# Kernel optimization log

Hardware: AMD Instinct MI355X
Metric: run time of the kernel (lower is better)

## Reference

```python
import jax, jax.numpy as jnp
import numpy as np

HIDDEN = 1024
HEADS = 16
HEAD_DIM = HIDDEN // HEADS  # 64; softmax scale uses head_dim per SeqAttention(hidden_size=head_dim)


def setup_inputs() -> dict:
    key = jax.random.key(0)
    ks = jax.random.split(key, 7)
    B, M = 2, 2048
    s = 1.0 / np.sqrt(HIDDEN)
    return {
        "query": jax.random.normal(ks[0], (B, M, HIDDEN), jnp.float32),
        "key": jax.random.normal(ks[1], (B, M, HIDDEN), jnp.float32),
        "value": jax.random.normal(ks[2], (B, M, HIDDEN), jnp.float32),
        "Wq": jax.random.normal(ks[3], (HIDDEN, HIDDEN), jnp.float32) * s,
        "Wk": jax.random.normal(ks[4], (HIDDEN, HIDDEN), jnp.float32) * s,
        "Wv": jax.random.normal(ks[5], (HIDDEN, HIDDEN), jnp.float32) * s,
        "Wo": jax.random.normal(ks[6], (HIDDEN, HIDDEN), jnp.float32) * s,
    }


def _split_heads(x):
    # [B, T, H*D] -> [B, H, T, D]
    B, T, _ = x.shape
    return x.reshape(B, T, HEADS, HEAD_DIM).transpose(0, 2, 1, 3)


def reference(query, key, value, Wq, Wk, Wv, Wo):
    # nn.Linear(bias=False): y = x @ W.T
    q = _split_heads(query @ Wq.T)  # [B,H,M,D]
    k = _split_heads(key @ Wk.T)    # [B,H,N,D]
    v = _split_heads(value @ Wv.T)  # [B,H,N,D]
    scale = 1.0 / jnp.sqrt(jnp.asarray(HEAD_DIM, q.dtype))
    attn = jnp.einsum("bhmd,bhnd->bhmn", q, k) * scale
    attn = jax.nn.softmax(attn, axis=-1)
    out = jnp.einsum("bhmn,bhnd->bhmd", attn, v)  # [B,H,M,D]
    B, H, M, D = out.shape
    out = out.transpose(0, 2, 1, 3).reshape(B, M, H * D)
    return out @ Wo.T
```

## Files before the change

kernel.cpp:

```cpp
#include <hip/hip_runtime.h>

typedef __bf16 bf16;
typedef __bf16 bf16x2 __attribute__((ext_vector_type(2)));
typedef __bf16 bf16x8 __attribute__((ext_vector_type(8)));
typedef float  f32x4  __attribute__((ext_vector_type(4)));
typedef float  f32x16 __attribute__((ext_vector_type(16)));
typedef unsigned int u32;
typedef unsigned int u32x4 __attribute__((ext_vector_type(4)));

typedef __attribute__((address_space(1))) unsigned int gu32;
typedef __attribute__((address_space(3))) unsigned int lu32;

__device__ __forceinline__ void llds16(const void* g, void* l) {
  __builtin_amdgcn_global_load_lds((gu32*)g, (lu32*)l, 16, 0, 0);
}

__device__ __forceinline__ void cvt8(const float* __restrict__ src,
                                     bf16* __restrict__ dst, int i) {
  const float4* s4 = (const float4*)src;
  float4 a = s4[i * 2 + 0];
  float4 c = s4[i * 2 + 1];
  bf16x8 o;
  o[0] = (bf16)a.x; o[1] = (bf16)a.y; o[2] = (bf16)a.z; o[3] = (bf16)a.w;
  o[4] = (bf16)c.x; o[5] = (bf16)c.y; o[6] = (bf16)c.z; o[7] = (bf16)c.w;
  ((bf16x8*)dst)[i] = o;
}

__global__ __launch_bounds__(256) void cvt_bf16(const float* __restrict__ src,
                                                bf16* __restrict__ dst, int n8) {
  int i = blockIdx.x * blockDim.x + threadIdx.x;
  if (i < n8) cvt8(src, dst, i);
}

__global__ __launch_bounds__(256) void cvt_all(const float* __restrict__ w0,
                                               const float* __restrict__ w1,
                                               const float* __restrict__ w2,
                                               const float* __restrict__ w3,
                                               const float* __restrict__ x0,
                                               const float* __restrict__ x1,
                                               const float* __restrict__ x2,
                                               bf16* __restrict__ wdst,
                                               bf16* __restrict__ xdst) {
  const int b = blockIdx.x;
  if (b < 2048) {
    const int which = b >> 9;
    const float* src = (which == 0) ? w0 : (which == 1) ? w1 : (which == 2) ? w2 : w3;
    const int i = (b & 511) * 256 + threadIdx.x;
    cvt8(src, wdst + (size_t)which * (1u << 20), i);
  } else {
    const int b2 = b - 2048;
    const int which = b2 >> 11;
    const float* src = (which == 0) ? x0 : (which == 1) ? x1 : x2;
    const int i = (b2 & 2047) * 256 + threadIdx.x;
    cvt8(src, xdst + (size_t)which * (4u << 20), i);
  }
}

__global__ __launch_bounds__(256) void gemm_qkv(const bf16* __restrict__ A0,
                                                const bf16* __restrict__ A1,
                                                const bf16* __restrict__ A2,
                                                const bf16* __restrict__ Wb,
                                                bf16* __restrict__ qb,
                                                bf16* __restrict__ kb,
                                                bf16* __restrict__ vb,
                                                int zoff) {
  constexpr int K = 1024, BM = 128, BN = 128, BK = 32, NT = K / BK;
  __shared__ bf16 Alds[2][BM * BK];
  __shared__ bf16 Blds[2][BN * BK];
  const int t = threadIdx.x, w = t >> 6, l = t & 63;
  const int lr = l & 15, lg = l >> 4;
  const int bm = blockIdx.x * BM, bn = blockIdx.y * BN;
  const int z = blockIdx.z + zoff;
  const bf16* A = (z == 0) ? A0 : (z == 1) ? A1 : A2;
  const bf16* W = Wb + (size_t)z * (1u << 20);
  const int wm = (w >> 1) * 64, wn = (w & 1) * 64;

  f32x4 acc[4][4] = {};

  auto stage = [&](int buf, int kt) {
    const int k0 = kt * BK;
#pragma unroll
    for (int i = 0; i < 2; ++i) {
      int idx = i * 256 + t;
      int row = idx >> 2, kb2 = (idx & 3) * 16;
      llds16((const char*)A + ((size_t)(bm + row) * K + k0) * 2 + kb2,
             (char*)(&Alds[buf][0]) + (i * 4 + w) * 1024);
    }
#pragma unroll
    for (int i = 0; i < 2; ++i) {
      int idx = i * 256 + t;
      int row = idx >> 2, kb2 = (idx & 3) * 16;
      llds16((const char*)W + ((size_t)(bn + row) * K + k0) * 2 + kb2,
             (char*)(&Blds[buf][0]) + (i * 4 + w) * 1024);
    }
  };

  stage(0, 0);
  for (int kt = 0; kt < NT; ++kt) {
    __syncthreads();
    if (kt + 1 < NT) stage((kt + 1) & 1, kt + 1);
    const int cur = kt & 1;
    bf16x8 af[4], bfr[4];
#pragma unroll
    for (int i = 0; i < 4; ++i)
      af[i] = *(const bf16x8*)(&Alds[cur][(wm + i * 16 + lr) * BK + lg * 8]);
#pragma unroll
    for (int j = 0; j < 4; ++j)
      bfr[j] = *(const bf16x8*)(&Blds[cur][(wn + j * 16 + lr) * BK + lg * 8]);
    __builtin_amdgcn_s_setprio(1);
#pragma unroll
    for (int i = 0; i < 4; ++i)
#pragma unroll
      for (int j = 0; j < 4; ++j)
        acc[i][j] = __builtin_amdgcn_mfma_f32_16x16x32_bf16(af[i], bfr[j], acc[i][j], 0, 0, 0);
    __builtin_amdgcn_s_setprio(0);
  }

  bf16* Cout = (z == 0) ? qb : (z == 1) ? kb : vb;
  const float osc = (z == 0) ? 0.1803368801f : 1.0f;
#pragma unroll
  for (int i = 0; i < 4; ++i) {
#pragma unroll
    for (int j = 0; j < 4; ++j) {
#pragma unroll
      for (int r = 0; r < 4; ++r) {
        const int gm = bm + wm + i * 16 + lg * 4 + r;
        const int n  = bn + wn + j * 16 + lr;
        const int b = gm >> 11, m = gm & 2047;
        const int h = n >> 6, d = n & 63;
        const size_t off = (z < 2)
            ? ((size_t)((b * 16 + h) * 2048 + m) * 64 + d)
            : ((size_t)((b * 16 + h) * 64 + d) * 2048 + m);
        Cout[off] = (bf16)(acc[i][j][r] * osc);
      }
    }
  }
}

__global__ __launch_bounds__(256) void gemm_out(const bf16* __restrict__ A,
                                                const bf16* __restrict__ Bw,
                                                float* __restrict__ Cout) {
  constexpr int N = 1024, K = 1024;
  constexpr int BM = 128, BN = 64, BK = 32;
  __shared__ bf16 Alds[2][BM * BK];
  __shared__ bf16 Blds[2][BN * BK];
  const int t = threadIdx.x;
  const int w = t >> 6, l = t & 63;
  const int lr = l & 15, lg = l >> 4;
  const int bm = blockIdx.x * BM, bn = blockIdx.y * BN;
  const int wm = (w >> 1) * 64, wn = (w & 1) * 32;

  f32x4 acc[4][2] = {};

  auto stage = [&](int buf, int kt) {
    const int k0 = kt * BK;
#pragma unroll
    for (int i = 0; i < 2; ++i) {
      int idx = i * 256 + t;
      int row = idx >> 2, kb = (idx & 3) * 16;
      const char* g = (const char*)A + ((size_t)(bm + row) * K + k0) * 2 + kb;
      llds16(g, (char*)(&Alds[buf][0]) + (i * 4 + w) * 1024);
    }
    {
      int row = t >> 2, kb = (t & 3) * 16;
      const char* g = (const char*)Bw + ((size_t)(bn + row) * K + k0) * 2 + kb;
      llds16(g, (char*)(&Blds[buf][0]) + w * 1024);
    }
  };

  stage(0, 0);
  constexpr int NT = K / BK;
  for (int kt = 0; kt < NT; ++kt) {
    __syncthreads();
    if (kt + 1 < NT) stage((kt + 1) & 1, kt + 1);
    const int cur = kt & 1;
    bf16x8 af[4], bfr[2];
#pragma unroll
    for (int i = 0; i < 4; ++i)
      af[i] = *(const bf16x8*)(&Alds[cur][(wm + i * 16 + lr) * BK + lg * 8]);
#pragma unroll
    for (int j = 0; j < 2; ++j)
      bfr[j] = *(const bf16x8*)(&Blds[cur][(wn + j * 16 + lr) * BK + lg * 8]);
    __builtin_amdgcn_s_setprio(1);
#pragma unroll
    for (int i = 0; i < 4; ++i)
#pragma unroll
      for (int j = 0; j < 2; ++j)
        acc[i][j] = __builtin_amdgcn_mfma_f32_16x16x32_bf16(af[i], bfr[j], acc[i][j], 0, 0, 0);
    __builtin_amdgcn_s_setprio(0);
  }

#pragma unroll
  for (int i = 0; i < 4; ++i)
#pragma unroll
    for (int j = 0; j < 2; ++j)
#pragma unroll
      for (int r = 0; r < 4; ++r) {
        const int gm = bm + wm + i * 16 + lg * 4 + r;
        const int n  = bn + wn + j * 16 + lr;
        Cout[(size_t)gm * N + n] = acc[i][j][r];
      }
}

__global__ __launch_bounds__(128) void attn_fwd(const bf16* __restrict__ Qb,
                                                const bf16* __restrict__ Kb,
                                                const bf16* __restrict__ Vt,
                                                bf16* __restrict__ Out) {
  constexpr int Mlen = 2048, KVB = 64, NTT = Mlen / KVB;
  __shared__ bf16 Klds[2][KVB * 64];
  __shared__ bf16 Vlds[2][64 * KVB];
  const int t = threadIdx.x, w = t >> 6, l = t & 63;
  const int l31 = l & 31, hi = l >> 5;
  const int orig = blockIdx.y * 32 + blockIdx.x;
  const int wg = (orig & 7) * 128 + (orig >> 3);
  const int bh = wg >> 5;
  const int qr = (wg & 31) * 64 + w * 32;
  const int key = (l31 & 7) << 4;

  const bf16* qbase = Qb + ((size_t)bh * Mlen + qr + l31) * 64;
  bf16x8 qf[4];
#pragma unroll
  for (int dks = 0; dks < 4; ++dks)
    qf[dks] = *(const bf16x8*)(qbase + dks * 16 + hi * 8);

  f32x16 acco0 = {}, acco1 = {};
  float lsum = 0.f;

  const char* kTile0 = (const char*)Kb + (size_t)bh * Mlen * 64 * 2;
  const char* vBase  = (const char*)Vt + (size_t)bh * 64 * Mlen * 2;

  auto stageKV = [&](int buf, int tile) {
    const int kv0 = tile * KVB;
#pragma unroll
    for (int i = 0; i < 4; ++i) {
      int idx = i * 128 + t;
      int L = idx * 16;
      int row = L >> 7;
      int inner = (L & 127) ^ ((row & 7) << 4);
      llds16(kTile0 + (size_t)(kv0 + row) * 128 + inner,
             (char*)(&Klds[buf][0]) + (i * 2 + w) * 1024);
    }
#pragma unroll
    for (int i = 0; i < 4; ++i) {
      int idx = i * 128 + t;
      int L = idx * 16;
      int d = L >> 7;
      int inner = (L & 127) ^ ((d & 7) << 4);
      llds16(vBase + (size_t)d * (Mlen * 2) + kv0 * 2 + inner,
             (char*)(&Vlds[buf][0]) + (i * 2 + w) * 1024);
    }
  };

  stageKV(0, 0);
  for (int tile = 0; tile < NTT; ++tile) {
    __syncthreads();
    if (tile + 1 < NTT) stageKV((tile + 1) & 1, tile + 1);
    const int cur = tile & 1;
    const char* kb_ = (const char*)(&Klds[cur][0]);
    const char* vb_ = (const char*)(&Vlds[cur][0]);

#pragma unroll
    for (int kvb = 0; kvb < 2; ++kvb) {
      f32x16 s = {};
      __builtin_amdgcn_s_setprio(1);
#pragma unroll
      for (int dks = 0; dks < 4; ++dks) {
        const int addr = (kvb * 32 + l31) * 128 + ((dks * 32 + hi * 16) ^ key);
        bf16x8 kf = *(const bf16x8*)(kb_ + addr);
        s = __builtin_amdgcn_mfma_f32_32x32x16_bf16(kf, qf[dks], s, 0, 0, 0);
      }
      __builtin_amdgcn_s_setprio(0);

      u32 wrd[8];
      float ts = 0.f;
#pragma unroll
      for (int e2 = 0; e2 < 8; ++e2) {
        const float p0 = __builtin_amdgcn_exp2f(s[2 * e2]);
        const float p1 = __builtin_amdgcn_exp2f(s[2 * e2 + 1]);
        ts += p0 + p1;
        bf16x2 pk; pk[0] = (bf16)p0; pk[1] = (bf16)p1;
        wrd[e2] = __builtin_bit_cast(u32, pk);
      }
      lsum += ts;

      __builtin_amdgcn_s_setprio(1);
#pragma unroll
      for (int ks = 0; ks < 2; ++ks) {
        auto sw0 = __builtin_amdgcn_permlane32_swap(wrd[4 * ks + 0], wrd[4 * ks + 2], false, false);
        auto sw1 = __builtin_amdgcn_permlane32_swap(wrd[4 * ks + 1], wrd[4 * ks + 3], false, false);
        u32x4 fv;
        fv[0] = (u32)sw0[0]; fv[1] = (u32)sw1[0];
        fv[2] = (u32)sw0[1]; fv[3] = (u32)sw1[1];
        const bf16x8 pa = __builtin_bit_cast(bf16x8, fv);
        const int va0 = (0 * 32 + l31) * 128 + ((kvb * 64 + ks * 32 + hi * 16) ^ key);
        const int va1 = (1 * 32 + l31) * 128 + ((kvb * 64 + ks * 32 + hi * 16) ^ key);
        bf16x8 vf0 = *(const bf16x8*)(vb_ + va0);
        bf16x8 vf1 = *(const bf16x8*)(vb_ + va1);
        acco0 = __builtin_amdgcn_mfma_f32_32x32x16_bf16(pa, vf0, acco0, 0, 0, 0);
        acco1 = __builtin_amdgcn_mfma_f32_32x32x16_bf16(pa, vf1, acco1, 0, 0, 0);
      }
      __builtin_amdgcn_s_setprio(0);
    }
  }

  float lf = lsum + __shfl_xor(lsum, 32, 64);
  const float inv = 1.0f / lf;
  const int b = bh >> 4, h = bh & 15;
#pragma unroll
  for (int e = 0; e < 16; ++e) {
    const int ql = (e & 3) + 8 * (e >> 2) + 4 * hi;
    const float iv = __shfl(inv, ql, 64);
    const size_t row = (size_t)(b * 2048 + qr + ql) * 1024 + h * 64;
    Out[row + l31]      = (bf16)(acco0[e] * iv);
    Out[row + 32 + l31] = (bf16)(acco1[e] * iv);
  }
}

extern "C" void kernel_launch(void* const* d_in, const int* in_sizes, int n_in,
                              void* d_out, int out_size, void* d_ws, size_t ws_size,
                              hipStream_t stream) {
  const float* q  = (const float*)d_in[0];
  const float* k  = (const float*)d_in[1];
  const float* v  = (const float*)d_in[2];
  const float* Wq = (const float*)d_in[3];
  const float* Wk = (const float*)d_in[4];
  const float* Wv = (const float*)d_in[5];
  const float* Wo = (const float*)d_in[6];

  char* ws = (char*)d_ws;
  const dim3 cb(256);

  if (ws_size >= ((size_t)56 << 20)) {
    bf16* Wb = (bf16*)ws;
    bf16* Xq = (bf16*)(ws + (8u  << 20));
    bf16* Xk = (bf16*)(ws + (16u << 20));
    bf16* Xv = (bf16*)(ws + (24u << 20));
    bf16* qb = (bf16*)(ws + (32u << 20));
    bf16* kb = (bf16*)(ws + (40u << 20));
    bf16* vb = (bf16*)(ws + (48u << 20));
    bf16* Xa = (bf16*)(ws + (8u  << 20));

    cvt_all<<<8192, cb, 0, stream>>>(Wq, Wk, Wv, Wo, q, k, v, Wb, Xq);
    gemm_qkv<<<dim3(32, 8, 3), cb, 0, stream>>>(Xq, Xk, Xv, Wb, qb, kb, vb, 0);
    attn_fwd<<<dim3(32, 32), dim3(128), 0, stream>>>(qb, kb, vb, Xa);
    gemm_out<<<dim3(32, 16), cb, 0, stream>>>(Xa, Wb + 3 * (1u << 20), (float*)d_out);
  } else {
    bf16* Wb = (bf16*)ws;
    bf16* X  = (bf16*)(ws + (8u  << 20));
    bf16* qb = (bf16*)(ws + (16u << 20));
    bf16* kb = (bf16*)(ws + (24u << 20));
    bf16* vb = (bf16*)(ws + (32u << 20));
    bf16* Xa = (bf16*)(ws + (8u  << 20));

    cvt_all<<<2048, cb, 0, stream>>>(Wq, Wk, Wv, Wo, q, k, v, Wb, Wb);
    cvt_bf16<<<2048, cb, 0, stream>>>(q, X, 524288);
    gemm_qkv<<<dim3(32, 8, 1), cb, 0, stream>>>(X, X, X, Wb, qb, kb, vb, 0);
    cvt_bf16<<<2048, cb, 0, stream>>>(k, X, 524288);
    gemm_qkv<<<dim3(32, 8, 1), cb, 0, stream>>>(X, X, X, Wb, qb, kb, vb, 1);
    cvt_bf16<<<2048, cb, 0, stream>>>(v, X, 524288);
    gemm_qkv<<<dim3(32, 8, 1), cb, 0, stream>>>(X, X, X, Wb, qb, kb, vb, 2);
    attn_fwd<<<dim3(32, 32), dim3(128), 0, stream>>>(qb, kb, vb, Xa);
    gemm_out<<<dim3(32, 16), cb, 0, stream>>>(Xa, Wb + 3 * (1u << 20), (float*)d_out);
  }
}
```

Before: 140.5 us.

## Split attention KV range in two and add a combine kernel

The attention kernel now splits each query tile's key/value range into two halves. This doubles the grid to 2048 workgroups and halves the loop length in each one. Each half writes an unnormalised bf16 partial output plus its row sum to workspace, and a new combine kernel adds the halves, normalises them and writes the head-interleaved layout. The aim is more parallelism and better CU occupancy, paid for by an extra launch, extra global traffic for the partials and bf16 rounding of the unnormalised partials.

Measured after the change: 147.2 us. +4.8%, slower.

```diff
diff --git a/kernel.cpp b/kernel.cpp
--- a/kernel.cpp
+++ b/kernel.cpp
@@ -202,19 +202,28 @@
       }
 }
 
+template <int SPLIT>
 __global__ __launch_bounds__(128) void attn_fwd(const bf16* __restrict__ Qb,
                                                 const bf16* __restrict__ Kb,
                                                 const bf16* __restrict__ Vt,
-                                                bf16* __restrict__ Out) {
-  constexpr int Mlen = 2048, KVB = 64, NTT = Mlen / KVB;
+                                                bf16* __restrict__ Out,
+                                                float* __restrict__ Lp) {
+  constexpr int Mlen = 2048, KVB = 64;
+  constexpr int NTT = (SPLIT == 2) ? 16 : 32;
   __shared__ bf16 Klds[2][KVB * 64];
   __shared__ bf16 Vlds[2][64 * KVB];
   const int t = threadIdx.x, w = t >> 6, l = t & 63;
   const int l31 = l & 31, hi = l >> 5;
-  const int orig = blockIdx.y * 32 + blockIdx.x;
-  const int wg = (orig & 7) * 128 + (orig >> 3);
-  const int bh = wg >> 5;
-  const int qr = (wg & 31) * 64 + w * 32;
+  const int orig = blockIdx.x;
+  int bh, half, qr;
+  if (SPLIT == 2) {
+    const int wg = (orig & 7) * 256 + (orig >> 3);
+    bh = wg >> 6; half = (wg >> 5) & 1; qr = (wg & 31) * 64 + w * 32;
+  } else {
+    const int wg = (orig & 7) * 128 + (orig >> 3);
+    bh = wg >> 5; half = 0; qr = (wg & 31) * 64 + w * 32;
+  }
+  const int kvbase = half * 1024;
   const int key = (l31 & 7) << 4;
 
   const bf16* qbase = Qb + ((size_t)bh * Mlen + qr + l31) * 64;
@@ -230,7 +239,7 @@
   const char* vBase  = (const char*)Vt + (size_t)bh * 64 * Mlen * 2;
 
   auto stageKV = [&](int buf, int tile) {
-    const int kv0 = tile * KVB;
+    const int kv0 = kvbase + tile * KVB;
 #pragma unroll
     for (int i = 0; i < 4; ++i) {
       int idx = i * 128 + t;
@@ -304,16 +313,48 @@
   }
 
   float lf = lsum + __shfl_xor(lsum, 32, 64);
-  const float inv = 1.0f / lf;
-  const int b = bh >> 4, h = bh & 15;
-#pragma unroll
-  for (int e = 0; e < 16; ++e) {
-    const int ql = (e & 3) + 8 * (e >> 2) + 4 * hi;
-    const float iv = __shfl(inv, ql, 64);
-    const size_t row = (size_t)(b * 2048 + qr + ql) * 1024 + h * 64;
-    Out[row + l31]      = (bf16)(acco0[e] * iv);
-    Out[row + 32 + l31] = (bf16)(acco1[e] * iv);
-  }
+  if (SPLIT == 2) {
+    const size_t obase = (size_t)(half * 32 + bh) * Mlen;
+    if (hi == 0) Lp[obase + qr + l31] = lf;
+#pragma unroll
+    for (int e = 0; e < 16; ++e) {
+      const int ql = (e & 3) + 8 * (e >> 2) + 4 * hi;
+      const size_t row = (obase + qr + ql) * 64;
+      Out[row + l31]      = (bf16)acco0[e];
+      Out[row + 32 + l31] = (bf16)acco1[e];
+    }
+  } else {
+    const float inv = 1.0f / lf;
+    const int b = bh >> 4, h = bh & 15;
+#pragma unroll
+    for (int e = 0; e < 16; ++e) {
+      const int ql = (e & 3) + 8 * (e >> 2) + 4 * hi;
+      const float iv = __shfl(inv, ql, 64);
+      const size_t row = (size_t)(b * 2048 + qr + ql) * 1024 + h * 64;
+      Out[row + l31]      = (bf16)(acco0[e] * iv);
+      Out[row + 32 + l31] = (bf16)(acco1[e] * iv);
+    }
+  }
+}
+
+__global__ __launch_bounds__(256) void combine(const bf16* __restrict__ O,
+                                               const float* __restrict__ Lp,
+                                               bf16* __restrict__ Xa) {
+  const int g = blockIdx.x * 256 + threadIdx.x;
+  const int d8 = g & 7;
+  const int q  = (g >> 3) & 2047;
+  const int bh = g >> 14;
+  const size_t i0 = ((size_t)bh * 2048 + q) * 8 + d8;
+  const size_t i1 = ((size_t)(32 + bh) * 2048 + q) * 8 + d8;
+  bf16x8 a = ((const bf16x8*)O)[i0];
+  bf16x8 b = ((const bf16x8*)O)[i1];
+  const float inv = 1.0f / (Lp[bh * 2048 + q] + Lp[(32 + bh) * 2048 + q]);
+  bf16x8 o;
+#pragma unroll
+  for (int i = 0; i < 8; ++i)
+    o[i] = (bf16)(((float)a[i] + (float)b[i]) * inv);
+  const size_t row = (size_t)(bh >> 4) * 2048 + q;
+  ((bf16x8*)Xa)[(row * 1024 + (size_t)(bh & 15) * 64 + d8 * 8) / 8] = o;
 }
 
 extern "C" void kernel_launch(void* const* d_in, const int* in_sizes, int n_in,
@@ -331,18 +372,21 @@
   const dim3 cb(256);
 
   if (ws_size >= ((size_t)56 << 20)) {
-    bf16* Wb = (bf16*)ws;
-    bf16* Xq = (bf16*)(ws + (8u  << 20));
-    bf16* Xk = (bf16*)(ws + (16u << 20));
-    bf16* Xv = (bf16*)(ws + (24u << 20));
-    bf16* qb = (bf16*)(ws + (32u << 20));
-    bf16* kb = (bf16*)(ws + (40u << 20));
-    bf16* vb = (bf16*)(ws + (48u << 20));
-    bf16* Xa = (bf16*)(ws + (8u  << 20));
+    bf16*  Wb = (bf16*)ws;
+    bf16*  Xq = (bf16*)(ws + (8u  << 20));
+    bf16*  Xk = (bf16*)(ws + (16u << 20));
+    bf16*  Xv = (bf16*)(ws + (24u << 20));
+    bf16*  qb = (bf16*)(ws + (32u << 20));
+    bf16*  kb = (bf16*)(ws + (40u << 20));
+    bf16*  vb = (bf16*)(ws + (48u << 20));
+    bf16*  Op = (bf16*)(ws + (8u  << 20));
+    float* Lp = (float*)(ws + (24u << 20));
+    bf16*  Xa = (bf16*)(ws + (32u << 20));
 
     cvt_all<<<8192, cb, 0, stream>>>(Wq, Wk, Wv, Wo, q, k, v, Wb, Xq);
     gemm_qkv<<<dim3(32, 8, 3), cb, 0, stream>>>(Xq, Xk, Xv, Wb, qb, kb, vb, 0);
-    attn_fwd<<<dim3(32, 32), dim3(128), 0, stream>>>(qb, kb, vb, Xa);
+    attn_fwd<2><<<2048, dim3(128), 0, stream>>>(qb, kb, vb, Op, Lp);
+    combine<<<2048, cb, 0, stream>>>(Op, Lp, Xa);
     gemm_out<<<dim3(32, 16), cb, 0, stream>>>(Xa, Wb + 3 * (1u << 20), (float*)d_out);
   } else {
     bf16* Wb = (bf16*)ws;
@@ -359,7 +403,7 @@
     gemm_qkv<<<dim3(32, 8, 1), cb, 0, stream>>>(X, X, X, Wb, qb, kb, vb, 1);
     cvt_bf16<<<2048, cb, 0, stream>>>(v, X, 524288);
     gemm_qkv<<<dim3(32, 8, 1), cb, 0, stream>>>(X, X, X, Wb, qb, kb, vb, 2);
-    attn_fwd<<<dim3(32, 32), dim3(128), 0, stream>>>(qb, kb, vb, Xa);
+    attn_fwd<1><<<1024, dim3(128), 0, stream>>>(qb, kb, vb, Xa, nullptr);
     gemm_out<<<dim3(32, 16), cb, 0, stream>>>(Xa, Wb + 3 * (1u << 20), (float*)d_out);
   }
 }
```

## Restructure attention to 4-wave blocks with triple-buffered KV and single barrier

Applied to the files above, without the earlier changes.

The attention kernel now runs 256-thread blocks covering 128 query rows, so each K/V tile staged in LDS is shared by four waves instead of two. This halves the number of global K/V loads per query. It also moves from double to triple buffering with an explicit vmcnt wait and a single barrier per tile, which lets the next tile's loads overlap compute without a second sync. Each iteration now processes both 32-key halves at once with interleaved MFMAs to expose more independent work. In exchange, register pressure and LDS usage per block rise, and the grid shrinks to 512 blocks.

New measurement: 131.8 us. -6.2%, faster.

```diff
diff --git a/kernel.cpp b/kernel.cpp
--- a/kernel.cpp
+++ b/kernel.cpp
@@ -202,19 +202,19 @@
       }
 }
 
-__global__ __launch_bounds__(128) void attn_fwd(const bf16* __restrict__ Qb,
+__global__ __launch_bounds__(256) void attn_fwd(const bf16* __restrict__ Qb,
                                                 const bf16* __restrict__ Kb,
                                                 const bf16* __restrict__ Vt,
                                                 bf16* __restrict__ Out) {
   constexpr int Mlen = 2048, KVB = 64, NTT = Mlen / KVB;
-  __shared__ bf16 Klds[2][KVB * 64];
-  __shared__ bf16 Vlds[2][64 * KVB];
+  __shared__ bf16 Klds[3][KVB * 64];
+  __shared__ bf16 Vlds[3][64 * KVB];
   const int t = threadIdx.x, w = t >> 6, l = t & 63;
   const int l31 = l & 31, hi = l >> 5;
-  const int orig = blockIdx.y * 32 + blockIdx.x;
-  const int wg = (orig & 7) * 128 + (orig >> 3);
-  const int bh = wg >> 5;
-  const int qr = (wg & 31) * 64 + w * 32;
+  const int orig = blockIdx.x;
+  const int wg = (orig & 7) * 64 + (orig >> 3);
+  const int bh = wg >> 4;
+  const int qr = (wg & 15) * 128 + w * 32;
   const int key = (l31 & 7) << 4;
 
   const bf16* qbase = Qb + ((size_t)bh * Mlen + qr + l31) * 64;
@@ -232,75 +232,93 @@
   auto stageKV = [&](int buf, int tile) {
     const int kv0 = tile * KVB;
 #pragma unroll
-    for (int i = 0; i < 4; ++i) {
-      int idx = i * 128 + t;
+    for (int i = 0; i < 2; ++i) {
+      int idx = i * 256 + t;
       int L = idx * 16;
       int row = L >> 7;
       int inner = (L & 127) ^ ((row & 7) << 4);
       llds16(kTile0 + (size_t)(kv0 + row) * 128 + inner,
-             (char*)(&Klds[buf][0]) + (i * 2 + w) * 1024);
-    }
-#pragma unroll
-    for (int i = 0; i < 4; ++i) {
-      int idx = i * 128 + t;
+             (char*)(&Klds[buf][0]) + (i * 4 + w) * 1024);
+    }
+#pragma unroll
+    for (int i = 0; i < 2; ++i) {
+      int idx = i * 256 + t;
       int L = idx * 16;
       int d = L >> 7;
       int inner = (L & 127) ^ ((d & 7) << 4);
       llds16(vBase + (size_t)d * (Mlen * 2) + kv0 * 2 + inner,
-             (char*)(&Vlds[buf][0]) + (i * 2 + w) * 1024);
+             (char*)(&Vlds[buf][0]) + (i * 4 + w) * 1024);
     }
   };
 
   stageKV(0, 0);
+  int bufc = 0;
   for (int tile = 0; tile < NTT; ++tile) {
-    __syncthreads();
-    if (tile + 1 < NTT) stageKV((tile + 1) & 1, tile + 1);
-    const int cur = tile & 1;
-    const char* kb_ = (const char*)(&Klds[cur][0]);
-    const char* vb_ = (const char*)(&Vlds[cur][0]);
-
-#pragma unroll
-    for (int kvb = 0; kvb < 2; ++kvb) {
-      f32x16 s = {};
-      __builtin_amdgcn_s_setprio(1);
-#pragma unroll
-      for (int dks = 0; dks < 4; ++dks) {
-        const int addr = (kvb * 32 + l31) * 128 + ((dks * 32 + hi * 16) ^ key);
-        bf16x8 kf = *(const bf16x8*)(kb_ + addr);
-        s = __builtin_amdgcn_mfma_f32_32x32x16_bf16(kf, qf[dks], s, 0, 0, 0);
-      }
-      __builtin_amdgcn_s_setprio(0);
-
-      u32 wrd[8];
-      float ts = 0.f;
-#pragma unroll
-      for (int e2 = 0; e2 < 8; ++e2) {
-        const float p0 = __builtin_amdgcn_exp2f(s[2 * e2]);
-        const float p1 = __builtin_amdgcn_exp2f(s[2 * e2 + 1]);
-        ts += p0 + p1;
-        bf16x2 pk; pk[0] = (bf16)p0; pk[1] = (bf16)p1;
-        wrd[e2] = __builtin_bit_cast(u32, pk);
-      }
-      lsum += ts;
-
-      __builtin_amdgcn_s_setprio(1);
-#pragma unroll
-      for (int ks = 0; ks < 2; ++ks) {
-        auto sw0 = __builtin_amdgcn_permlane32_swap(wrd[4 * ks + 0], wrd[4 * ks + 2], false, false);
-        auto sw1 = __builtin_amdgcn_permlane32_swap(wrd[4 * ks + 1], wrd[4 * ks + 3], false, false);
-        u32x4 fv;
-        fv[0] = (u32)sw0[0]; fv[1] = (u32)sw1[0];
-        fv[2] = (u32)sw0[1]; fv[3] = (u32)sw1[1];
-        const bf16x8 pa = __builtin_bit_cast(bf16x8, fv);
-        const int va0 = (0 * 32 + l31) * 128 + ((kvb * 64 + ks * 32 + hi * 16) ^ key);
-        const int va1 = (1 * 32 + l31) * 128 + ((kvb * 64 + ks * 32 + hi * 16) ^ key);
-        bf16x8 vf0 = *(const bf16x8*)(vb_ + va0);
-        bf16x8 vf1 = *(const bf16x8*)(vb_ + va1);
-        acco0 = __builtin_amdgcn_mfma_f32_32x32x16_bf16(pa, vf0, acco0, 0, 0, 0);
-        acco1 = __builtin_amdgcn_mfma_f32_32x32x16_bf16(pa, vf1, acco1, 0, 0, 0);
-      }
-      __builtin_amdgcn_s_setprio(0);
-    }
+    const int bufn = (bufc == 2) ? 0 : bufc + 1;
+    if (tile + 1 < NTT) {
+      stageKV(bufn, tile + 1);
+      asm volatile("s_waitcnt vmcnt(4)" ::: "memory");
+    } else {
+      asm volatile("s_waitcnt vmcnt(0)" ::: "memory");
+    }
+    __builtin_amdgcn_s_barrier();
+    __builtin_amdgcn_sched_barrier(0);
+    const char* kb_ = (const char*)(&Klds[bufc][0]);
+    const char* vb_ = (const char*)(&Vlds[bufc][0]);
+
+    f32x16 s0 = {}, s1 = {};
+    __builtin_amdgcn_s_setprio(1);
+#pragma unroll
+    for (int dks = 0; dks < 4; ++dks) {
+      const int a0 = (0 * 32 + l31) * 128 + ((dks * 32 + hi * 16) ^ key);
+      const int a1 = (1 * 32 + l31) * 128 + ((dks * 32 + hi * 16) ^ key);
+      bf16x8 kf0 = *(const bf16x8*)(kb_ + a0);
+      bf16x8 kf1 = *(const bf16x8*)(kb_ + a1);
+      s0 = __builtin_amdgcn_mfma_f32_32x32x16_bf16(kf0, qf[dks], s0, 0, 0, 0);
+      s1 = __builtin_amdgcn_mfma_f32_32x32x16_bf16(kf1, qf[dks], s1, 0, 0, 0);
+    }
+    __builtin_amdgcn_s_setprio(0);
+
+    u32 wrd0[8], wrd1[8];
+    float ts = 0.f;
+#pragma unroll
+    for (int e2 = 0; e2 < 8; ++e2) {
+      const float p00 = __builtin_amdgcn_exp2f(s0[2 * e2]);
+      const float p01 = __builtin_amdgcn_exp2f(s0[2 * e2 + 1]);
+      const float p10 = __builtin_amdgcn_exp2f(s1[2 * e2]);
+      const float p11 = __builtin_amdgcn_exp2f(s1[2 * e2 + 1]);
+      ts += (p00 + p01) + (p10 + p11);
+      bf16x2 k0; k0[0] = (bf16)p00; k0[1] = (bf16)p01;
+      bf16x2 k1; k1[0] = (bf16)p10; k1[1] = (bf16)p11;
+      wrd0[e2] = __builtin_bit_cast(u32, k0);
+      wrd1[e2] = __builtin_bit_cast(u32, k1);
+    }
+    lsum += ts;
+
+    __builtin_amdgcn_s_setprio(1);
+#pragma unroll
+    for (int ks = 0; ks < 2; ++ks) {
+      auto sa0 = __builtin_amdgcn_permlane32_swap(wrd0[4 * ks + 0], wrd0[4 * ks + 2], false, false);
+      auto sa1 = __builtin_amdgcn_permlane32_swap(wrd0[4 * ks + 1], wrd0[4 * ks + 3], false, false);
+      auto sb0 = __builtin_amdgcn_permlane32_swap(wrd1[4 * ks + 0], wrd1[4 * ks + 2], false, false);
+      auto sb1 = __builtin_amdgcn_permlane32_swap(wrd1[4 * ks + 1], wrd1[4 * ks + 3], false, false);
+      u32x4 fa, fb;
+      fa[0] = (u32)sa0[0]; fa[1] = (u32)sa1[0]; fa[2] = (u32)sa0[1]; fa[3] = (u32)sa1[1];
+      fb[0] = (u32)sb0[0]; fb[1] = (u32)sb1[0]; fb[2] = (u32)sb0[1]; fb[3] = (u32)sb1[1];
+      const bf16x8 pa = __builtin_bit_cast(bf16x8, fa);
+      const bf16x8 pb = __builtin_bit_cast(bf16x8, fb);
+      const int c0 = (ks * 32 + hi * 16);
+      bf16x8 va0 = *(const bf16x8*)(vb_ + (0 * 32 + l31) * 128 + ((0 * 64 + c0) ^ key));
+      bf16x8 va1 = *(const bf16x8*)(vb_ + (1 * 32 + l31) * 128 + ((0 * 64 + c0) ^ key));
+      bf16x8 vb0 = *(const bf16x8*)(vb_ + (0 * 32 + l31) * 128 + ((1 * 64 + c0) ^ key));
+      bf16x8 vb1 = *(const bf16x8*)(vb_ + (1 * 32 + l31) * 128 + ((1 * 64 + c0) ^ key));
+      acco0 = __builtin_amdgcn_mfma_f32_32x32x16_bf16(pa, va0, acco0, 0, 0, 0);
+      acco1 = __builtin_amdgcn_mfma_f32_32x32x16_bf16(pa, va1, acco1, 0, 0, 0);
+      acco0 = __builtin_amdgcn_mfma_f32_32x32x16_bf16(pb, vb0, acco0, 0, 0, 0);
+      acco1 = __builtin_amdgcn_mfma_f32_32x32x16_bf16(pb, vb1, acco1, 0, 0, 0);
+    }
+    __builtin_amdgcn_s_setprio(0);
+    bufc = bufn;
   }
 
   float lf = lsum + __shfl_xor(lsum, 32, 64);
@@ -342,7 +360,7 @@
 
     cvt_all<<<8192, cb, 0, stream>>>(Wq, Wk, Wv, Wo, q, k, v, Wb, Xq);
     gemm_qkv<<<dim3(32, 8, 3), cb, 0, stream>>>(Xq, Xk, Xv, Wb, qb, kb, vb, 0);
-    attn_fwd<<<dim3(32, 32), dim3(128), 0, stream>>>(qb, kb, vb, Xa);
+    attn_fwd<<<512, cb, 0, stream>>>(qb, kb, vb, Xa);
     gemm_out<<<dim3(32, 16), cb, 0, stream>>>(Xa, Wb + 3 * (1u << 20), (float*)d_out);
   } else {
     bf16* Wb = (bf16*)ws;
@@ -359,7 +377,7 @@
     gemm_qkv<<<dim3(32, 8, 1), cb, 0, stream>>>(X, X, X, Wb, qb, kb, vb, 1);
     cvt_bf16<<<2048, cb, 0, stream>>>(v, X, 524288);
     gemm_qkv<<<dim3(32, 8, 1), cb, 0, stream>>>(X, X, X, Wb, qb, kb, vb, 2);
-    attn_fwd<<<dim3(32, 32), dim3(128), 0, stream>>>(qb, kb, vb, Xa);
+    attn_fwd<<<512, cb, 0, stream>>>(qb, kb, vb, Xa);
     gemm_out<<<dim3(32, 16), cb, 0, stream>>>(Xa, Wb + 3 * (1u << 20), (float*)d_out);
   }
 }
```
